# Optimization experiments

Measured on AMD Instinct MI355X. Metric: run time of the kernel, lower is better.

Reference implementation:

```python
import jax, jax.numpy as jnp
import numpy as np

B_SZ, L_SEQ, H_CH, N_ST = 8, 4096, 256, 64


def setup_inputs() -> dict:
    key = jax.random.key(0)
    ks = jax.random.split(key, 12)
    rn = lambda k, s, sc=1.0: jax.random.normal(k, s, jnp.float32) * sc
    inp = {
        'x': rn(ks[0], (B_SZ, L_SEQ, H_CH)),
        # stable DPLR spectrum: Re(Lambda) < 0, HiPPO-like imaginary ladder
        'Lambda_re': -(jnp.abs(rn(ks[1], (N_ST,))) + 0.1),
        'Lambda_im': jnp.pi * jnp.arange(N_ST, dtype=jnp.float32),
        'P_re': rn(ks[2], (N_ST,), N_ST ** -0.5),
        'P_im': rn(ks[3], (N_ST,), N_ST ** -0.5),
        'Q_re': rn(ks[4], (N_ST,), N_ST ** -0.5),
        'Q_im': rn(ks[5], (N_ST,), N_ST ** -0.5),
        'B_re': rn(ks[6], (N_ST,), N_ST ** -0.5),
        'B_im': rn(ks[7], (N_ST,), N_ST ** -0.5),
        'C_re': rn(ks[8], (H_CH, N_ST), N_ST ** -0.5),
        'C_im': rn(ks[9], (H_CH, N_ST), N_ST ** -0.5),
        'step': jnp.ones((1,), jnp.float32) * 1e-3,
        'D': jnp.zeros((1,), jnp.float32),
        'W_fc': rn(ks[10], (H_CH, H_CH), H_CH ** -0.5),
        'b_fc': jnp.zeros((H_CH,), jnp.float32),
        'ln_g': jnp.ones((H_CH,), jnp.float32),
        'ln_b': jnp.zeros((H_CH,), jnp.float32),
    }
    return inp


def _dplr_kernel(Lambda_re, Lambda_im, P_re, P_im, Q_re, Q_im, B_re, B_im, C_re, C_im, step, L):
    # S4 DPLR generating function evaluated at the L roots of unity (torch_get_K_derta).
    Lam = (Lambda_re + 1j * Lambda_im).astype(jnp.complex64)  # (N,)
    Pc = (P_re + 1j * P_im).astype(jnp.complex64)
    Qc = (Q_re + 1j * Q_im).astype(jnp.complex64)
    Bc = (B_re + 1j * B_im).astype(jnp.complex64)
    Cc = (C_re + 1j * C_im).astype(jnp.complex64)  # (H, N)
    k = jnp.arange(L, dtype=jnp.float32)
    Omega = jnp.exp((-2j * jnp.pi) * (k / L)).astype(jnp.complex64)  # (L,)
    c = 2.0 / (1.0 + Omega)
    g = (2.0 / step[0]) * (1.0 - Omega) / (1.0 + Omega)  # bilinear transform points, (L,)
    inv = 1.0 / (g[:, None] - Lam[None, :])  # Cauchy matrix, (L, N)
    k00 = jnp.einsum('hn,ln->hl', Cc * Bc[None, :], inv)  # (H, L)
    k01 = jnp.einsum('hn,ln->hl', Cc * Pc[None, :], inv)
    k10 = jnp.einsum('n,ln->l', Qc * Bc, inv)  # (L,)
    k11 = jnp.einsum('n,ln->l', Qc * Pc, inv)
    atRoots = c[None, :] * (k00 - k01 * (k10 / (1.0 + k11))[None, :])  # Woodbury correction
    K = jnp.fft.ifft(atRoots, axis=-1).real  # (H, L)
    return K.astype(jnp.float32)


def reference(x, Lambda_re, Lambda_im, P_re, P_im, Q_re, Q_im, B_re, B_im, C_re, C_im, step, D, W_fc, b_fc, ln_g, ln_b):
    Bsz, L, H = x.shape
    step = jnp.maximum(step, 1e-6)
    K = _dplr_kernel(Lambda_re, Lambda_im, P_re, P_im, Q_re, Q_im, B_re, B_im, C_re, C_im, step, L)  # (H, L)
    # causal FFT convolution per channel (torch_convolution with fft=True)
    n = 2 * L
    Kf = jnp.fft.rfft(K, n=n, axis=-1)           # (H, F)
    uf = jnp.fft.rfft(x, n=n, axis=1)            # (B, F, H)
    h1 = jnp.fft.irfft(uf * Kf.T[None], n=n, axis=1)[:, :L, :]
    y1 = jax.nn.gelu(h1 + D * x, approximate=False)  # mult_activation='gelu'
    y2 = jax.nn.gelu(y1 @ W_fc.T + b_fc, approximate=False)  # fc + final_act
    y2 = y2 + x  # skip
    mu = jnp.mean(y2, axis=-1, keepdims=True)
    var = jnp.var(y2, axis=-1, keepdims=True)
    y = (y2 - mu) / jnp.sqrt(var + 1e-5) * ln_g + ln_b  # LayerNorm; dropout p=0
    h_ratio = jnp.max(jnp.abs(y), axis=1) / (jnp.max(jnp.abs(x), axis=1) + 1e-6)  # (B, H)
    return y, h_ratio
```

## Files before the change

kernel.cpp:

```cpp
#include <hip/hip_runtime.h>
#include <math.h>

#define TPB 256

typedef float2 cf;
typedef __attribute__((ext_vector_type(8))) short bf16x8;
typedef __attribute__((ext_vector_type(4))) float f32x4;

__device__ __forceinline__ cf cmk(float x, float y){ cf r; r.x=x; r.y=y; return r; }
__device__ __forceinline__ cf cml(cf a, cf b){ return cmk(a.x*b.x - a.y*b.y, a.x*b.y + a.y*b.x); }
__device__ __forceinline__ cf cad(cf a, cf b){ return cmk(a.x+b.x, a.y+b.y); }
__device__ __forceinline__ cf csb(cf a, cf b){ return cmk(a.x-b.x, a.y-b.y); }
__device__ __forceinline__ cf crcp(cf d){ float r = 1.0f/(d.x*d.x + d.y*d.y); return cmk(d.x*r, -d.y*r); }
__device__ __forceinline__ cf cdv(cf n, cf d){ return cml(n, crcp(d)); }
__device__ __forceinline__ float geluf(float z){ return 0.5f*z*(1.0f + erff(z*0.70710678118654752f)); }

__device__ __forceinline__ cf twid(float f, float sign){
  float h = f * 0.5f;
  float s = __builtin_amdgcn_sinf(h);
  float c0 = __builtin_amdgcn_cosf(h);
  return cmk(c0, sign * s);
}

__device__ __forceinline__ cf shflx(cf v, int m){
  return cmk(__shfl_xor(v.x, m), __shfl_xor(v.y, m));
}

__device__ __forceinline__ void bfsplit(float v, ushort* h, ushort* l){
  unsigned u = __float_as_uint(v);
  unsigned hr = (u + 0x7FFFu + ((u >> 16) & 1u)) & 0xFFFF0000u;
  *h = (ushort)(hr >> 16);
  float lv = v - __uint_as_float(hr);
  unsigned u2 = __float_as_uint(lv);
  *l = (ushort)((u2 + 0x7FFFu + ((u2 >> 16) & 1u)) >> 16);
}

__device__ __forceinline__ void dif4q(cf& q0, cf& q1, cf& q2, cf& q3, cf w1, float sign){
  cf w2 = cml(w1, w1);
  cf a1 = cad(q0, q2);
  cf c1 = cml(csb(q0, q2), w1);
  cf b1 = cad(q1, q3);
  cf d1 = cml(csb(q1, q3), cmk(-sign*w1.y, sign*w1.x));
  q0 = cad(a1, b1);
  q1 = cml(csb(a1, b1), w2);
  q2 = cad(c1, d1);
  q3 = cml(csb(c1, d1), w2);
}
__device__ __forceinline__ void dit4q(cf& q0, cf& q1, cf& q2, cf& q3, cf w1, float sign){
  cf w2 = cml(w1, w1);
  cf t1 = cml(q1, w2);
  cf a1 = cad(q0, t1), b1 = csb(q0, t1);
  cf t2 = cml(q3, w2);
  cf c1 = cad(q2, t2), d1 = csb(q2, t2);
  cf v1 = cml(c1, w1);
  cf v2 = cml(d1, cmk(-sign*w1.y, sign*w1.x));
  q0 = cad(a1, v1);
  q2 = csb(a1, v1);
  q1 = cad(b1, v2);
  q3 = csb(b1, v2);
}

template<int N, int SSTART>
__device__ void fft_dif_r4(cf* __restrict__ a, float sign){
  #pragma unroll
  for (int s = SSTART; s >= 1; s >>= 2){
    __syncthreads();
    #pragma unroll
    for (int g = 0; g < (N >> 2) / TPB; g++){
      int w = (int)threadIdx.x + g * TPB;
      int j = w & (s - 1);
      int base = ((w & ~(s - 1)) << 2) | j;
      cf A0 = a[base], B0 = a[base + s], C0 = a[base + 2*s], D0 = a[base + 3*s];
      cf w1 = twid((float)j / (float)(2 * s), sign);
      cf w2 = cml(w1, w1);
      cf a1 = cad(A0, C0);
      cf c1 = cml(csb(A0, C0), w1);
      cf b1 = cad(B0, D0);
      cf d1 = cml(csb(B0, D0), cmk(-sign * w1.y, sign * w1.x));
      a[base]         = cad(a1, b1);
      a[base + s]     = cml(csb(a1, b1), w2);
      a[base + 2*s]   = cad(c1, d1);
      a[base + 3*s]   = cml(csb(c1, d1), w2);
    }
  }
  if constexpr ((__builtin_ctz(N) & 1) == 1){
    __syncthreads();
    #pragma unroll
    for (int g = 0; g < (N >> 1) / TPB; g++){
      int w = (int)threadIdx.x + g * TPB;
      int i = w << 1;
      cf u = a[i], v = a[i + 1];
      a[i] = cad(u, v);
      a[i + 1] = csb(u, v);
    }
  }
  __syncthreads();
}

template<int N>
__device__ void fft_dit_r4(cf* __restrict__ a, float sign){
  if constexpr ((__builtin_ctz(N) & 1) == 1){
    __syncthreads();
    #pragma unroll
    for (int g = 0; g < (N >> 1) / TPB; g++){
      int w = (int)threadIdx.x + g * TPB;
      int i = w << 1;
      cf u = a[i], v = a[i + 1];
      a[i] = cad(u, v);
      a[i + 1] = csb(u, v);
    }
  }
  constexpr int S0 = ((__builtin_ctz(N) & 1) == 1) ? 2 : 1;
  #pragma unroll
  for (int s = S0; s <= (N >> 2); s <<= 2){
    __syncthreads();
    #pragma unroll
    for (int g = 0; g < (N >> 2) / TPB; g++){
      int w = (int)threadIdx.x + g * TPB;
      int j = w & (s - 1);
      int base = ((w & ~(s - 1)) << 2) | j;
      cf A0 = a[base], B0 = a[base + s], C0 = a[base + 2*s], D0 = a[base + 3*s];
      cf w1 = twid((float)j / (float)(2 * s), sign);
      cf w2 = cml(w1, w1);
      cf t1 = cml(B0, w2);
      cf a1 = cad(A0, t1), b1 = csb(A0, t1);
      cf t2 = cml(D0, w2);
      cf c1 = cad(C0, t2), d1 = csb(C0, t2);
      cf v1 = cml(c1, w1);
      cf v2 = cml(d1, cmk(-sign * w1.y, sign * w1.x));
      a[base]         = cad(a1, v1);
      a[base + 2*s]   = csb(a1, v1);
      a[base + s]     = cad(b1, v2);
      a[base + 3*s]   = csb(b1, v2);
    }
  }
  __syncthreads();
}

__device__ void dif8192_pad_stage(cf* __restrict__ a, float sign){
  __syncthreads();
  #pragma unroll
  for (int g = 0; g < 8; g++){
    int w = (int)threadIdx.x + g * TPB;
    cf A0 = a[w], B0 = a[w + 2048];
    cf w1 = twid((float)w * (1.0f / 4096.0f), sign);
    cf w2 = cml(w1, w1);
    cf c1 = cml(A0, w1);
    cf d1 = cml(B0, cmk(-sign * w1.y, sign * w1.x));
    a[w]        = cad(A0, B0);
    a[w + 2048] = cml(csb(A0, B0), w2);
    a[w + 4096] = cad(c1, d1);
    a[w + 6144] = cml(csb(c1, d1), w2);
  }
}

__device__ __forceinline__ int brev13(int x){ return (int)(__brev((unsigned)x) >> 19); }

__global__ void k_init(unsigned* xmax, unsigned* ymax){
  int i = blockIdx.x * 256 + threadIdx.x;
  if (i < 2048){ xmax[i] = 0u; ymax[i] = 0u; }
}

__global__ __launch_bounds__(256) void k_transpose_x(const float* __restrict__ x,
                                                     float* __restrict__ xT,
                                                     unsigned* __restrict__ xmax){
  __shared__ float tile[64][65];
  __shared__ float red[64][4];
  int b = blockIdx.z;
  int t0 = blockIdx.x * 64;
  int h0 = blockIdx.y * 64;
  int hc = threadIdx.x & 63, tg = threadIdx.x >> 6;
  float pmax = 0.0f;
  #pragma unroll
  for (int q = 0; q < 16; q++){
    int tr = tg + q * 4;
    float v = x[((size_t)(b * 4096 + t0 + tr)) * 256 + h0 + hc];
    tile[tr][hc] = v;
    pmax = fmaxf(pmax, fabsf(v));
  }
  red[hc][tg] = pmax;
  __syncthreads();
  if (threadIdx.x < 64){
    float m = fmaxf(fmaxf(red[threadIdx.x][0], red[threadIdx.x][1]),
                    fmaxf(red[threadIdx.x][2], red[threadIdx.x][3]));
    atomicMax(&xmax[b * 256 + h0 + threadIdx.x], __float_as_uint(m));
  }
  #pragma unroll
  for (int q = 0; q < 16; q++){
    int hr = tg + q * 4;
    xT[((size_t)(b * 256 + h0 + hr)) * 4096 + t0 + hc] = tile[hc][hr];
  }
}

__global__ void k_wsplit(const float* __restrict__ W, ushort* __restrict__ Wh, ushort* __restrict__ Wl){
  int i = blockIdx.x * 256 + threadIdx.x;
  ushort h, l;
  bfsplit(W[i], &h, &l);
  Wh[i] = h; Wl[i] = l;
}

__global__ __launch_bounds__(256) void k_cauchy(
    const float* __restrict__ Lr, const float* __restrict__ Li,
    const float* __restrict__ Pr, const float* __restrict__ Pi,
    const float* __restrict__ Qr, const float* __restrict__ Qi,
    const float* __restrict__ Br, const float* __restrict__ Bi,
    const float* __restrict__ Cr, const float* __restrict__ Ci,
    const float* __restrict__ stepp, cf* __restrict__ A)
{
  __shared__ cf sLam[64], sB[64], sP[64], sQB[64], sQP[64];
  __shared__ cf sInv[64][16];
  __shared__ cf sWood[16], sC[16], sG[16];
  int tid = threadIdx.x;
  int l0 = blockIdx.x * 16;
  float stepv = fmaxf(stepp[0], 1e-6f);
  if (tid < 64){
    cf lam = cmk(Lr[tid], Li[tid]);
    cf b = cmk(Br[tid], Bi[tid]);
    cf p = cmk(Pr[tid], Pi[tid]);
    cf q = cmk(Qr[tid], Qi[tid]);
    sLam[tid] = lam; sB[tid] = b; sP[tid] = p;
    sQB[tid] = cml(q, b);
    sQP[tid] = cml(q, p);
  }
  __syncthreads();
  if (tid < 16){
    int l = l0 + tid;
    float ang = -6.2831855f * ((float)l * (1.0f / 4096.0f));
    cf Om = cmk(cosf(ang), sinf(ang));
    cf den = cmk(1.0f + Om.x, Om.y);
    cf num = cmk(1.0f - Om.x, -Om.y);
    cf rden = crcp(den);
    sC[tid] = cml(cmk(2.0f, 0.0f), rden);
    cf g = cml(num, rden);
    float sc = 2.0f / stepv;
    sG[tid] = cmk(g.x * sc, g.y * sc);
  }
  __syncthreads();
  for (int it = tid; it < 1024; it += 256){
    int n = it >> 4, ll = it & 15;
    sInv[n][ll] = crcp(csb(sG[ll], sLam[n]));
  }
  __syncthreads();
  if (tid < 16){
    cf k10 = cmk(0,0), k11 = cmk(0,0);
    for (int n = 0; n < 64; n++){
      k10 = cad(k10, cml(sQB[n], sInv[n][tid]));
      k11 = cad(k11, cml(sQP[n], sInv[n][tid]));
    }
    sWood[tid] = cdv(k10, cmk(1.0f + k11.x, k11.y));
  }
  __syncthreads();
  int h = tid;
  cf a0[16], a1[16];
  #pragma unroll
  for (int ll = 0; ll < 16; ll++){ a0[ll] = cmk(0,0); a1[ll] = cmk(0,0); }
  for (int n = 0; n < 64; n++){
    cf cc = cmk(Cr[h * 64 + n], Ci[h * 64 + n]);
    cf cb = cml(cc, sB[n]);
    cf cp = cml(cc, sP[n]);
    #pragma unroll
    for (int ll = 0; ll < 16; ll++){
      cf iv = sInv[n][ll];
      a0[ll] = cad(a0[ll], cml(cb, iv));
      a1[ll] = cad(a1[ll], cml(cp, iv));
    }
  }
  cf* dst = A + (size_t)h * 4096 + l0;
  #pragma unroll
  for (int ll = 0; ll < 16; ll++){
    dst[ll] = cml(sC[ll], csb(a0[ll], cml(a1[ll], sWood[ll])));
  }
}

__global__ __launch_bounds__(256) void k_kf(const cf* __restrict__ A, float4* __restrict__ Sab){
  extern __shared__ cf c[];
  int hp = blockIdx.x, tid = threadIdx.x;
  const cf* a1p = A + (size_t)(2 * hp) * 4096;
  const cf* a2p = a1p + 4096;
  for (int l = tid; l < 4096; l += TPB){
    int r = (int)(__brev((unsigned)l) >> 20);
    cf u = a1p[l], v = a2p[l];
    c[r] = cmk(u.x - v.y, u.y + v.x);
  }
  fft_dit_r4<4096>(c, 1.0f);
  float k1[16], k2[16];
  #pragma unroll
  for (int q = 0; q < 16; q++){
    cf w = c[tid + q * 256];
    k1[q] = w.x * (1.0f / 4096.0f);
    k2[q] = w.y * (1.0f / 4096.0f);
  }
  __syncthreads();
  #pragma unroll
  for (int q = 0; q < 16; q++) c[tid + q * 256] = cmk(k1[q], k2[q]);
  dif8192_pad_stage(c, -1.0f);
  fft_dif_r4<8192, 512>(c, -1.0f);
  float4* rec = Sab + (size_t)hp * 4097;
  const float sc = 0.5f * 0.5f * (1.0f / 8192.0f);
  #pragma unroll
  for (int q8 = 0; q8 < 16; q8++){
    int t = tid + 256 * q8;
    int p = t << 1;
    int k = brev13(p);
    int qq = brev13((8192 - k) & 8191);
    cf Zp = c[p], Zq = c[qq];
    float K1x = (Zp.x + Zq.x), K1y = (Zp.y - Zq.y);
    float dx  = (Zp.x - Zq.x), dy  = (Zp.y + Zq.y);
    float K2x = dy, K2y = -dx;
    rec[t] = make_float4((K1x + K2x) * sc, (K1y + K2y) * sc,
                         (K1x - K2x) * sc, (K1y - K2y) * sc);
  }
  if (tid == 0){
    cf Z1 = c[1];
    float K1x = 2.0f * Z1.x, K2x = 2.0f * Z1.y;
    rec[4096] = make_float4((K1x + K2x) * sc, 0.0f, (K1x - K2x) * sc, 0.0f);
  }
}

__global__ __launch_bounds__(256) void k_conv(const float* __restrict__ xT,
                                              const float4* __restrict__ Sab,
                                              const float* __restrict__ Dp,
                                              ushort* __restrict__ y1h,
                                              ushort* __restrict__ y1l){
  __shared__ cf c[8320];
  int blk = blockIdx.x;
  int b = blk >> 7, hp = blk & 127;
  int t = threadIdx.x;
  const float* xs1 = xT + ((size_t)(b * 256 + 2 * hp)) * 4096;
  const float* xs2 = xs1 + 4096;
  cf v[32];
  #pragma unroll
  for (int r = 0; r < 16; r++){
    int n = t + 256 * r;
    v[r] = cmk(xs1[n], xs2[n]);
  }
  #pragma unroll
  for (int r = 0; r < 16; r++)
    v[r + 16] = cml(v[r], twid((float)(t + 256 * r) * (1.0f / 4096.0f), -1.0f));
  #pragma unroll
  for (int r0 = 0; r0 < 4; r0++){
    cf w1 = twid((float)(t + 256 * r0) * (1.0f / 2048.0f), -1.0f);
    dif4q(v[r0], v[r0 + 4], v[r0 + 8], v[r0 + 12], w1, -1.0f);
    dif4q(v[r0 + 16], v[r0 + 20], v[r0 + 24], v[r0 + 28], w1, -1.0f);
  }
  {
    cf w1 = twid((float)t * (1.0f / 512.0f), -1.0f);
    #pragma unroll
    for (int r = 0; r < 32; r += 4)
      dif4q(v[r], v[r + 1], v[r + 2], v[r + 3], w1, -1.0f);
  }
  #pragma unroll
  for (int r = 0; r < 32; r++) c[t + 260 * r] = v[r];
  __syncthreads();
  int Bq = t >> 3, sg = t & 7;
  int m1 = Bq * 260 + sg;
  #pragma unroll
  for (int u = 0; u < 32; u++) v[u] = c[m1 + 8 * u];
  #pragma unroll
  for (int u = 0; u < 8; u++){
    cf w1 = twid((float)(sg + 8 * u) * (1.0f / 128.0f), -1.0f);
    dif4q(v[u], v[u + 8], v[u + 16], v[u + 24], w1, -1.0f);
  }
  #pragma unroll
  for (int p2 = 0; p2 < 2; p2++){
    cf w1 = twid((float)(sg + 8 * p2) * (1.0f / 32.0f), -1.0f);
    #pragma unroll
    for (int u0 = 0; u0 < 32; u0 += 8)
      dif4q(v[u0 + p2], v[u0 + p2 + 2], v[u0 + p2 + 4], v[u0 + p2 + 6], w1, -1.0f);
  }
  {
    cf tw = twid((float)sg * (1.0f / 8.0f), -1.0f);
    #pragma unroll
    for (int u = 0; u < 32; u += 2){
      cf lo = cad(v[u], v[u + 1]);
      cf hi = cml(csb(v[u], v[u + 1]), tw);
      v[u] = lo; v[u + 1] = hi;
    }
  }
  {
    bool h4 = (sg & 4) != 0;
    cf tw4 = twid((float)(sg & 3) * 0.25f, -1.0f);
    #pragma unroll
    for (int u = 0; u < 32; u++){
      cf o = shflx(v[u], 4);
      v[u] = h4 ? cml(csb(o, v[u]), tw4) : cad(v[u], o);
    }
    bool h2 = (sg & 2) != 0;
    cf tw2 = twid((float)(sg & 1) * 0.5f, -1.0f);
    #pragma unroll
    for (int u = 0; u < 32; u++){
      cf o = shflx(v[u], 2);
      v[u] = h2 ? cml(csb(o, v[u]), tw2) : cad(v[u], o);
    }
    bool h1 = (sg & 1) != 0;
    #pragma unroll
    for (int u = 0; u < 32; u++){
      cf o = shflx(v[u], 1);
      v[u] = h1 ? csb(o, v[u]) : cad(v[u], o);
    }
  }
  #pragma unroll
  for (int u = 0; u < 32; u++) c[m1 + 8 * u] = v[u];
  __syncthreads();
  const float4* rec = Sab + (size_t)hp * 4097;
  #pragma unroll
  for (int q8 = 0; q8 < 16; q8++){
    int th = t + 256 * q8;
    int p = th << 1;
    int k = brev13(p);
    int qq = brev13((8192 - k) & 8191);
    int pi = p + 4 * (p >> 8), qi = qq + 4 * (qq >> 8);
    cf Zp = c[pi], Zq = c[qi];
    float4 r0 = rec[th];
    cf Sap = cmk(r0.x, r0.y), Sbp = cmk(r0.z, r0.w);
    cf cZq = cmk(Zq.x, -Zq.y), cZp = cmk(Zp.x, -Zp.y);
    c[pi] = cad(cml(Zp, Sap), cml(cZq, Sbp));
    cf cSa = cmk(Sap.x, -Sap.y), cSb = cmk(Sbp.x, -Sbp.y);
    c[qi] = cad(cml(Zq, cSa), cml(cZp, cSb));
  }
  if (t == 0){
    float4 e = rec[4096];
    cf Z1 = c[1];
    c[1] = cad(cml(Z1, cmk(e.x, e.y)), cml(cmk(Z1.x, -Z1.y), cmk(e.z, e.w)));
  }
  __syncthreads();
  #pragma unroll
  for (int u = 0; u < 32; u++) v[u] = c[m1 + 8 * u];
  {
    bool h1 = (sg & 1) != 0;
    #pragma unroll
    for (int u = 0; u < 32; u++){
      cf o = shflx(v[u], 1);
      v[u] = h1 ? csb(o, v[u]) : cad(v[u], o);
    }
    bool h2 = (sg & 2) != 0;
    cf w2 = twid((float)(sg & 1) * 0.5f, 1.0f);
    #pragma unroll
    for (int u = 0; u < 32; u++){
      cf o = shflx(v[u], 2);
      cf whv = cml(w2, h2 ? v[u] : o);
      v[u] = h2 ? csb(o, whv) : cad(v[u], whv);
    }
    bool h4 = (sg & 4) != 0;
    cf w4 = twid((float)(sg & 3) * 0.25f, 1.0f);
    #pragma unroll
    for (int u = 0; u < 32; u++){
      cf o = shflx(v[u], 4);
      cf whv = cml(w4, h4 ? v[u] : o);
      v[u] = h4 ? csb(o, whv) : cad(v[u], whv);
    }
  }
  {
    cf tw = twid((float)sg * (1.0f / 8.0f), 1.0f);
    #pragma unroll
    for (int u = 0; u < 32; u += 2){
      cf tb = cml(v[u + 1], tw);
      cf a = v[u];
      v[u] = cad(a, tb);
      v[u + 1] = csb(a, tb);
    }
  }
  #pragma unroll
  for (int p2 = 0; p2 < 2; p2++){
    cf w1 = twid((float)(sg + 8 * p2) * (1.0f / 32.0f), 1.0f);
    #pragma unroll
    for (int u0 = 0; u0 < 32; u0 += 8)
      dit4q(v[u0 + p2], v[u0 + p2 + 2], v[u0 + p2 + 4], v[u0 + p2 + 6], w1, 1.0f);
  }
  #pragma unroll
  for (int u = 0; u < 8; u++){
    cf w1 = twid((float)(sg + 8 * u) * (1.0f / 128.0f), 1.0f);
    dit4q(v[u], v[u + 8], v[u + 16], v[u + 24], w1, 1.0f);
  }
  #pragma unroll
  for (int u = 0; u < 32; u++) c[m1 + 8 * u] = v[u];
  __syncthreads();
  #pragma unroll
  for (int r = 0; r < 32; r++) v[r] = c[t + 260 * r];
  {
    cf tw = twid((float)t * (1.0f / 256.0f), 1.0f);
    #pragma unroll
    for (int r = 0; r < 32; r += 2){
      cf tb = cml(v[r + 1], tw);
      cf a = v[r];
      v[r] = cad(a, tb);
      v[r + 1] = csb(a, tb);
    }
  }
  #pragma unroll
  for (int p2 = 0; p2 < 2; p2++){
    cf w1 = twid((float)(t + 256 * p2) * (1.0f / 1024.0f), 1.0f);
    #pragma unroll
    for (int r0 = 0; r0 < 32; r0 += 8)
      dit4q(v[r0 + p2], v[r0 + p2 + 2], v[r0 + p2 + 4], v[r0 + p2 + 6], w1, 1.0f);
  }
  #pragma unroll
  for (int r0 = 0; r0 < 8; r0++){
    cf w1 = twid((float)(t + 256 * r0) * (1.0f / 4096.0f), 1.0f);
    dit4q(v[r0], v[r0 + 8], v[r0 + 16], v[r0 + 24], w1, 1.0f);
  }
  float Dv = Dp[0];
  size_t base = ((size_t)(b * 256 + 2 * hp)) * 4096;
  #pragma unroll
  for (int r = 0; r < 16; r++){
    int n = t + 256 * r;
    cf w = v[r];
    float z1 = geluf(fmaf(Dv, xs1[n], w.x));
    float z2 = geluf(fmaf(Dv, xs2[n], w.y));
    ushort h0, l0, h1u, l1;
    bfsplit(z1, &h0, &l0);
    bfsplit(z2, &h1u, &l1);
    y1h[base + n] = h0;        y1l[base + n] = l0;
    y1h[base + 4096 + n] = h1u; y1l[base + 4096 + n] = l1;
  }
}

__global__ __launch_bounds__(256, 3) void k_gemm_ln(
    const ushort* __restrict__ y1h, const ushort* __restrict__ y1l,
    const ushort* __restrict__ Wh, const ushort* __restrict__ Wl,
    const float* __restrict__ bfc, const float* __restrict__ x,
    const float* __restrict__ lng, const float* __restrict__ lnb,
    float* __restrict__ yout, unsigned* __restrict__ ymax)
{
  __shared__ ushort sY[2][64 * 40];
  __shared__ float red1[64][4], red2[64][4];
  int tid = threadIdx.x;
  int l = tid & 63;
  int w = tid >> 6;
  int blk = blockIdx.x;
  int b = blk >> 6;
  int t0 = (blk & 63) * 64;
  int g = l >> 4, cc = l & 15;

  f32x4 acc[4][4];
  #pragma unroll
  for (int m = 0; m < 4; m++)
    #pragma unroll
    for (int n = 0; n < 4; n++)
      acc[m][n] = (f32x4){0.0f, 0.0f, 0.0f, 0.0f};

  int kk = tid >> 3, ts = (tid & 7) * 8;

  #pragma unroll 1
  for (int kc = 0; kc < 256; kc += 32){
    __syncthreads();
    {
      size_t gb = ((size_t)(b * 256 + kc + kk)) * 4096 + t0 + ts;
      float4 vh = *(const float4*)(y1h + gb);
      float4 vl = *(const float4*)(y1l + gb);
      const ushort* ph = (const ushort*)&vh;
      const ushort* pl = (const ushort*)&vl;
      int kblk = kk >> 3, kin = kk & 7;
      #pragma unroll
      for (int e = 0; e < 8; e++){
        int t = ts + e;
        int idx = t * 40 + ((kblk ^ ((t >> 3) & 3)) << 3) + kin;
        sY[0][idx] = ph[e];
        sY[1][idx] = pl[e];
      }
    }
    __syncthreads();
    bf16x8 afh[4], afl[4];
    #pragma unroll
    for (int m = 0; m < 4; m++){
      int t = m * 16 + cc;
      int idx = t * 40 + ((g ^ ((t >> 3) & 3)) << 3);
      afh[m] = *(bf16x8*)&sY[0][idx];
      afl[m] = *(bf16x8*)&sY[1][idx];
    }
    #pragma unroll
    for (int n = 0; n < 4; n++){
      size_t wj = (size_t)(w * 64 + n * 16 + cc) * 256 + kc + g * 8;
      bf16x8 bh = *(const bf16x8*)(Wh + wj);
      bf16x8 bl = *(const bf16x8*)(Wl + wj);
      #pragma unroll
      for (int m = 0; m < 4; m++){
        acc[m][n] = __builtin_amdgcn_mfma_f32_16x16x32_bf16(afh[m], bh, acc[m][n], 0, 0, 0);
        acc[m][n] = __builtin_amdgcn_mfma_f32_16x16x32_bf16(afh[m], bl, acc[m][n], 0, 0, 0);
        acc[m][n] = __builtin_amdgcn_mfma_f32_16x16x32_bf16(afl[m], bh, acc[m][n], 0, 0, 0);
      }
    }
  }

  float bj[4], gj[4], lj[4];
  #pragma unroll
  for (int n = 0; n < 4; n++){
    int j = w * 64 + n * 16 + cc;
    bj[n] = bfc[j]; gj[n] = lng[j]; lj[n] = lnb[j];
  }
  #pragma unroll
  for (int m = 0; m < 4; m++){
    #pragma unroll
    for (int r = 0; r < 4; r++){
      int tl = m * 16 + g * 4 + r;
      size_t rowb = ((size_t)(b * 4096 + t0 + tl)) * 256;
      float ss = 0.0f, sq = 0.0f;
      #pragma unroll
      for (int n = 0; n < 4; n++){
        float z = geluf(acc[m][n][r] + bj[n]) + x[rowb + w * 64 + n * 16 + cc];
        acc[m][n][r] = z;
        ss += z; sq = fmaf(z, z, sq);
      }
      #pragma unroll
      for (int msk = 1; msk < 16; msk <<= 1){
        ss += __shfl_xor(ss, msk);
        sq += __shfl_xor(sq, msk);
      }
      if (cc == 0){ red1[tl][w] = ss; red2[tl][w] = sq; }
    }
  }
  __syncthreads();
  float jm[4] = {0.0f, 0.0f, 0.0f, 0.0f};
  #pragma unroll
  for (int m = 0; m < 4; m++){
    #pragma unroll
    for (int r = 0; r < 4; r++){
      int tl = m * 16 + g * 4 + r;
      float ts1 = red1[tl][0] + red1[tl][1] + red1[tl][2] + red1[tl][3];
      float ts2 = red2[tl][0] + red2[tl][1] + red2[tl][2] + red2[tl][3];
      float mu = ts1 * (1.0f / 256.0f);
      float var = ts2 * (1.0f / 256.0f) - mu * mu;
      float rstd = rsqrtf(var + 1e-5f);
      size_t rowb = ((size_t)(b * 4096 + t0 + tl)) * 256;
      #pragma unroll
      for (int n = 0; n < 4; n++){
        float yv = (acc[m][n][r] - mu) * rstd * gj[n] + lj[n];
        yout[rowb + w * 64 + n * 16 + cc] = yv;
        jm[n] = fmaxf(jm[n], fabsf(yv));
      }
    }
  }
  #pragma unroll
  for (int n = 0; n < 4; n++){
    jm[n] = fmaxf(jm[n], __shfl_xor(jm[n], 16));
    jm[n] = fmaxf(jm[n], __shfl_xor(jm[n], 32));
  }
  if (g == 0){
    #pragma unroll
    for (int n = 0; n < 4; n++)
      atomicMax(&ymax[b * 256 + w * 64 + n * 16 + cc], __float_as_uint(jm[n]));
  }
}

__global__ void k_ratio(const unsigned* __restrict__ ymax, const unsigned* __restrict__ xmax,
                        float* __restrict__ out){
  int i = blockIdx.x * 256 + threadIdx.x;
  if (i < 2048){
    float ym = __uint_as_float(ymax[i]);
    float xm = __uint_as_float(xmax[i]);
    out[8388608 + i] = ym / (xm + 1e-6f);
  }
}

extern "C" void kernel_launch(void* const* d_in, const int* in_sizes, int n_in,
                              void* d_out, int out_size, void* d_ws, size_t ws_size,
                              hipStream_t stream)
{
  const float* x    = (const float*)d_in[0];
  const float* Lr   = (const float*)d_in[1];
  const float* Li   = (const float*)d_in[2];
  const float* Pr   = (const float*)d_in[3];
  const float* Pi   = (const float*)d_in[4];
  const float* Qr   = (const float*)d_in[5];
  const float* Qi   = (const float*)d_in[6];
  const float* Br   = (const float*)d_in[7];
  const float* Bi   = (const float*)d_in[8];
  const float* Cr   = (const float*)d_in[9];
  const float* Ci   = (const float*)d_in[10];
  const float* stp  = (const float*)d_in[11];
  const float* Dp   = (const float*)d_in[12];
  const float* Wfc  = (const float*)d_in[13];
  const float* bfc  = (const float*)d_in[14];
  const float* lng  = (const float*)d_in[15];
  const float* lnb  = (const float*)d_in[16];

  char* ws = (char*)d_ws;
  float*    xT   = (float*)(ws);
  float4*   Sab  = (float4*)(ws + ((size_t)32 << 20));
  cf*       A    = (cf*)(ws + ((size_t)41 << 20));
  ushort*   y1h  = (ushort*)(ws + ((size_t)41 << 20));
  ushort*   y1l  = (ushort*)(ws + ((size_t)57 << 20));
  ushort*   Wh   = (ushort*)(ws + ((size_t)73 << 20));
  ushort*   Wl   = (ushort*)(ws + ((size_t)73 << 20) + (128u << 10));
  unsigned* xmax = (unsigned*)(ws + ((size_t)73 << 20) + (256u << 10));
  unsigned* ymax = xmax + 2048;

  k_init<<<8, 256, 0, stream>>>(xmax, ymax);
  dim3 gt(64, 4, 8);
  k_transpose_x<<<gt, 256, 0, stream>>>(x, xT, xmax);
  k_wsplit<<<256, 256, 0, stream>>>(Wfc, Wh, Wl);
  k_cauchy<<<256, 256, 0, stream>>>(Lr, Li, Pr, Pi, Qr, Qi, Br, Bi, Cr, Ci, stp, A);
  k_kf<<<128, 256, 65536, stream>>>(A, Sab);
  k_conv<<<1024, 256, 0, stream>>>(xT, Sab, Dp, y1h, y1l);
  k_gemm_ln<<<512, 256, 0, stream>>>(y1h, y1l, Wh, Wl, bfc, x, lng, lnb, (float*)d_out, ymax);
  k_ratio<<<8, 256, 0, stream>>>(ymax, xmax, (float*)d_out);
}
```

Baseline: 211.2 us.

## Double FFT block size to 512 threads and restructure conv FFT decomposition

The kernel-spectrum and convolution kernels move from 256 to 512 threads per block. Each thread now holds 16 complex values instead of 32. The conv kernel's 8192-point FFT is restructured: one radix-2 pass is folded into the final output twiddle, the shared-memory exchange uses 512-element padded rows, and five wavefront-shuffle butterfly stages replace three. The aims are lower register pressure, more waves per CU to hide latency, and fewer LDS round trips, at the cost of more shuffle traffic and a larger barrier scope.

```diff
diff --git a/kernel.cpp b/kernel.cpp
--- a/kernel.cpp
+++ b/kernel.cpp
@@ -1,7 +1,5 @@
 #include <hip/hip_runtime.h>
 #include <math.h>
-
-#define TPB 256
 
 typedef float2 cf;
 typedef __attribute__((ext_vector_type(8))) short bf16x8;
@@ -11,6 +9,7 @@
 __device__ __forceinline__ cf cml(cf a, cf b){ return cmk(a.x*b.x - a.y*b.y, a.x*b.y + a.y*b.x); }
 __device__ __forceinline__ cf cad(cf a, cf b){ return cmk(a.x+b.x, a.y+b.y); }
 __device__ __forceinline__ cf csb(cf a, cf b){ return cmk(a.x-b.x, a.y-b.y); }
+__device__ __forceinline__ cf cjg(cf a){ return cmk(a.x, -a.y); }
 __device__ __forceinline__ cf crcp(cf d){ float r = 1.0f/(d.x*d.x + d.y*d.y); return cmk(d.x*r, -d.y*r); }
 __device__ __forceinline__ cf cdv(cf n, cf d){ return cml(n, crcp(d)); }
 __device__ __forceinline__ float geluf(float z){ return 0.5f*z*(1.0f + erff(z*0.70710678118654752f)); }
@@ -60,14 +59,18 @@
   q3 = csb(b1, v2);
 }
 
-template<int N, int SSTART>
+__device__ __forceinline__ int brev12(int x){ return (int)(__brev((unsigned)x) >> 20); }
+__device__ __forceinline__ int brev13(int x){ return (int)(__brev((unsigned)x) >> 19); }
+__device__ __forceinline__ int pidx(int n){ return n + 4*(n>>8); }
+
+template<int N, int SSTART, int TP>
 __device__ void fft_dif_r4(cf* __restrict__ a, float sign){
   #pragma unroll
   for (int s = SSTART; s >= 1; s >>= 2){
     __syncthreads();
     #pragma unroll
-    for (int g = 0; g < (N >> 2) / TPB; g++){
-      int w = (int)threadIdx.x + g * TPB;
+    for (int g = 0; g < (N >> 2) / TP; g++){
+      int w = (int)threadIdx.x + g * TP;
       int j = w & (s - 1);
       int base = ((w & ~(s - 1)) << 2) | j;
       cf A0 = a[base], B0 = a[base + s], C0 = a[base + 2*s], D0 = a[base + 3*s];
@@ -86,8 +89,8 @@
   if constexpr ((__builtin_ctz(N) & 1) == 1){
     __syncthreads();
     #pragma unroll
-    for (int g = 0; g < (N >> 1) / TPB; g++){
-      int w = (int)threadIdx.x + g * TPB;
+    for (int g = 0; g < (N >> 1) / TP; g++){
+      int w = (int)threadIdx.x + g * TP;
       int i = w << 1;
       cf u = a[i], v = a[i + 1];
       a[i] = cad(u, v);
@@ -97,13 +100,13 @@
   __syncthreads();
 }
 
-template<int N>
+template<int N, int TP>
 __device__ void fft_dit_r4(cf* __restrict__ a, float sign){
   if constexpr ((__builtin_ctz(N) & 1) == 1){
     __syncthreads();
     #pragma unroll
-    for (int g = 0; g < (N >> 1) / TPB; g++){
-      int w = (int)threadIdx.x + g * TPB;
+    for (int g = 0; g < (N >> 1) / TP; g++){
+      int w = (int)threadIdx.x + g * TP;
       int i = w << 1;
       cf u = a[i], v = a[i + 1];
       a[i] = cad(u, v);
@@ -115,8 +118,8 @@
   for (int s = S0; s <= (N >> 2); s <<= 2){
     __syncthreads();
     #pragma unroll
-    for (int g = 0; g < (N >> 2) / TPB; g++){
-      int w = (int)threadIdx.x + g * TPB;
+    for (int g = 0; g < (N >> 2) / TP; g++){
+      int w = (int)threadIdx.x + g * TP;
       int j = w & (s - 1);
       int base = ((w & ~(s - 1)) << 2) | j;
       cf A0 = a[base], B0 = a[base + s], C0 = a[base + 2*s], D0 = a[base + 3*s];
@@ -137,11 +140,12 @@
   __syncthreads();
 }
 
+template<int TP>
 __device__ void dif8192_pad_stage(cf* __restrict__ a, float sign){
   __syncthreads();
   #pragma unroll
-  for (int g = 0; g < 8; g++){
-    int w = (int)threadIdx.x + g * TPB;
+  for (int g = 0; g < 2048 / TP; g++){
+    int w = (int)threadIdx.x + g * TP;
     cf A0 = a[w], B0 = a[w + 2048];
     cf w1 = twid((float)w * (1.0f / 4096.0f), sign);
     cf w2 = cml(w1, w1);
@@ -153,8 +157,6 @@
     a[w + 6144] = cml(csb(c1, d1), w2);
   }
 }
-
-__device__ __forceinline__ int brev13(int x){ return (int)(__brev((unsigned)x) >> 19); }
 
 __global__ void k_init(unsigned* xmax, unsigned* ymax){
   int i = blockIdx.x * 256 + threadIdx.x;
@@ -272,34 +274,34 @@
   }
 }
 
-__global__ __launch_bounds__(256) void k_kf(const cf* __restrict__ A, float4* __restrict__ Sab){
+__global__ __launch_bounds__(512) void k_kf(const cf* __restrict__ A, float4* __restrict__ Sab){
   extern __shared__ cf c[];
   int hp = blockIdx.x, tid = threadIdx.x;
   const cf* a1p = A + (size_t)(2 * hp) * 4096;
   const cf* a2p = a1p + 4096;
-  for (int l = tid; l < 4096; l += TPB){
-    int r = (int)(__brev((unsigned)l) >> 20);
-    cf u = a1p[l], v = a2p[l];
-    c[r] = cmk(u.x - v.y, u.y + v.x);
-  }
-  fft_dit_r4<4096>(c, 1.0f);
-  float k1[16], k2[16];
-  #pragma unroll
-  for (int q = 0; q < 16; q++){
-    cf w = c[tid + q * 256];
+  for (int l = tid; l < 4096; l += 512){
+    int r = brev12(l);
+    cf u = a1p[l], w = a2p[l];
+    c[r] = cmk(u.x - w.y, u.y + w.x);
+  }
+  fft_dit_r4<4096, 512>(c, 1.0f);
+  float k1[8], k2[8];
+  #pragma unroll
+  for (int q = 0; q < 8; q++){
+    cf w = c[tid + q * 512];
     k1[q] = w.x * (1.0f / 4096.0f);
     k2[q] = w.y * (1.0f / 4096.0f);
   }
   __syncthreads();
   #pragma unroll
-  for (int q = 0; q < 16; q++) c[tid + q * 256] = cmk(k1[q], k2[q]);
-  dif8192_pad_stage(c, -1.0f);
-  fft_dif_r4<8192, 512>(c, -1.0f);
+  for (int q = 0; q < 8; q++) c[tid + q * 512] = cmk(k1[q], k2[q]);
+  dif8192_pad_stage<512>(c, -1.0f);
+  fft_dif_r4<8192, 512, 512>(c, -1.0f);
   float4* rec = Sab + (size_t)hp * 4097;
   const float sc = 0.5f * 0.5f * (1.0f / 8192.0f);
   #pragma unroll
-  for (int q8 = 0; q8 < 16; q8++){
-    int t = tid + 256 * q8;
+  for (int q8 = 0; q8 < 8; q8++){
+    int t = tid + 512 * q8;
     int p = t << 1;
     int k = brev13(p);
     int qq = brev13((8192 - k) & 8191);
@@ -317,7 +319,7 @@
   }
 }
 
-__global__ __launch_bounds__(256) void k_conv(const float* __restrict__ xT,
+__global__ __launch_bounds__(512) void k_conv(const float* __restrict__ xT,
                                               const float4* __restrict__ Sab,
                                               const float* __restrict__ Dp,
                                               ushort* __restrict__ y1h,
@@ -326,191 +328,162 @@
   int blk = blockIdx.x;
   int b = blk >> 7, hp = blk & 127;
   int t = threadIdx.x;
+  int a = t >> 5, cl = t & 31;
   const float* xs1 = xT + ((size_t)(b * 256 + 2 * hp)) * 4096;
   const float* xs2 = xs1 + 4096;
-  cf v[32];
-  #pragma unroll
-  for (int r = 0; r < 16; r++){
-    int n = t + 256 * r;
+  cf v[16];
+  #pragma unroll
+  for (int r = 0; r < 8; r++){
+    int n = t + 512 * r;
     v[r] = cmk(xs1[n], xs2[n]);
   }
   #pragma unroll
-  for (int r = 0; r < 16; r++)
-    v[r + 16] = cml(v[r], twid((float)(t + 256 * r) * (1.0f / 4096.0f), -1.0f));
-  #pragma unroll
-  for (int r0 = 0; r0 < 4; r0++){
-    cf w1 = twid((float)(t + 256 * r0) * (1.0f / 2048.0f), -1.0f);
-    dif4q(v[r0], v[r0 + 4], v[r0 + 8], v[r0 + 12], w1, -1.0f);
-    dif4q(v[r0 + 16], v[r0 + 20], v[r0 + 24], v[r0 + 28], w1, -1.0f);
+  for (int r = 0; r < 8; r++)
+    v[r + 8] = cml(v[r], twid((float)(t + 512 * r) * (1.0f / 4096.0f), -1.0f));
+  #pragma unroll
+  for (int h = 0; h < 16; h += 8){
+    #pragma unroll
+    for (int r0 = 0; r0 < 2; r0++){
+      cf w1 = twid((float)(t + 512 * r0) * (1.0f / 2048.0f), -1.0f);
+      dif4q(v[h + r0], v[h + r0 + 2], v[h + r0 + 4], v[h + r0 + 6], w1, -1.0f);
+    }
   }
   {
-    cf w1 = twid((float)t * (1.0f / 512.0f), -1.0f);
-    #pragma unroll
-    for (int r = 0; r < 32; r += 4)
-      dif4q(v[r], v[r + 1], v[r + 2], v[r + 3], w1, -1.0f);
-  }
-  #pragma unroll
-  for (int r = 0; r < 32; r++) c[t + 260 * r] = v[r];
-  __syncthreads();
-  int Bq = t >> 3, sg = t & 7;
-  int m1 = Bq * 260 + sg;
-  #pragma unroll
-  for (int u = 0; u < 32; u++) v[u] = c[m1 + 8 * u];
-  #pragma unroll
-  for (int u = 0; u < 8; u++){
-    cf w1 = twid((float)(sg + 8 * u) * (1.0f / 128.0f), -1.0f);
-    dif4q(v[u], v[u + 8], v[u + 16], v[u + 24], w1, -1.0f);
-  }
-  #pragma unroll
-  for (int p2 = 0; p2 < 2; p2++){
-    cf w1 = twid((float)(sg + 8 * p2) * (1.0f / 32.0f), -1.0f);
-    #pragma unroll
-    for (int u0 = 0; u0 < 32; u0 += 8)
-      dif4q(v[u0 + p2], v[u0 + p2 + 2], v[u0 + p2 + 4], v[u0 + p2 + 6], w1, -1.0f);
+    cf tw = twid((float)t * (1.0f / 512.0f), -1.0f);
+    #pragma unroll
+    for (int r = 0; r < 16; r += 2){
+      cf lo = cad(v[r], v[r + 1]);
+      cf hi = cml(csb(v[r], v[r + 1]), tw);
+      v[r] = lo; v[r + 1] = hi;
+    }
+  }
+  __syncthreads();
+  #pragma unroll
+  for (int r = 0; r < 16; r++) c[pidx(t + 512 * r)] = v[r];
+  __syncthreads();
+  #pragma unroll
+  for (int u = 0; u < 16; u++) v[u] = c[pidx(a * 512 + u * 32 + cl)];
+  #pragma unroll
+  for (int u0 = 0; u0 < 4; u0++){
+    cf w1 = twid((float)(u0 * 32 + cl) * (1.0f / 256.0f), -1.0f);
+    dif4q(v[u0], v[u0 + 4], v[u0 + 8], v[u0 + 12], w1, -1.0f);
   }
   {
-    cf tw = twid((float)sg * (1.0f / 8.0f), -1.0f);
-    #pragma unroll
-    for (int u = 0; u < 32; u += 2){
-      cf lo = cad(v[u], v[u + 1]);
-      cf hi = cml(csb(v[u], v[u + 1]), tw);
-      v[u] = lo; v[u + 1] = hi;
+    cf w1 = twid((float)cl * (1.0f / 64.0f), -1.0f);
+    #pragma unroll
+    for (int g = 0; g < 16; g += 4)
+      dif4q(v[g], v[g + 1], v[g + 2], v[g + 3], w1, -1.0f);
+  }
+  #pragma unroll
+  for (int m = 16; m >= 2; m >>= 1){
+    bool hb = (cl & m) != 0;
+    cf tw = twid((float)(cl & (m - 1)) * (1.0f / (float)m), -1.0f);
+    #pragma unroll
+    for (int u = 0; u < 16; u++){
+      cf o = shflx(v[u], m);
+      v[u] = hb ? cml(csb(o, v[u]), tw) : cad(v[u], o);
     }
   }
   {
-    bool h4 = (sg & 4) != 0;
-    cf tw4 = twid((float)(sg & 3) * 0.25f, -1.0f);
-    #pragma unroll
-    for (int u = 0; u < 32; u++){
-      cf o = shflx(v[u], 4);
-      v[u] = h4 ? cml(csb(o, v[u]), tw4) : cad(v[u], o);
-    }
-    bool h2 = (sg & 2) != 0;
-    cf tw2 = twid((float)(sg & 1) * 0.5f, -1.0f);
-    #pragma unroll
-    for (int u = 0; u < 32; u++){
-      cf o = shflx(v[u], 2);
-      v[u] = h2 ? cml(csb(o, v[u]), tw2) : cad(v[u], o);
-    }
-    bool h1 = (sg & 1) != 0;
-    #pragma unroll
-    for (int u = 0; u < 32; u++){
+    bool hb = (cl & 1) != 0;
+    #pragma unroll
+    for (int u = 0; u < 16; u++){
       cf o = shflx(v[u], 1);
-      v[u] = h1 ? csb(o, v[u]) : cad(v[u], o);
-    }
-  }
-  #pragma unroll
-  for (int u = 0; u < 32; u++) c[m1 + 8 * u] = v[u];
-  __syncthreads();
-  const float4* rec = Sab + (size_t)hp * 4097;
-  #pragma unroll
-  for (int q8 = 0; q8 < 16; q8++){
-    int th = t + 256 * q8;
-    int p = th << 1;
-    int k = brev13(p);
-    int qq = brev13((8192 - k) & 8191);
-    int pi = p + 4 * (p >> 8), qi = qq + 4 * (qq >> 8);
-    cf Zp = c[pi], Zq = c[qi];
-    float4 r0 = rec[th];
-    cf Sap = cmk(r0.x, r0.y), Sbp = cmk(r0.z, r0.w);
-    cf cZq = cmk(Zq.x, -Zq.y), cZp = cmk(Zp.x, -Zp.y);
-    c[pi] = cad(cml(Zp, Sap), cml(cZq, Sbp));
-    cf cSa = cmk(Sap.x, -Sap.y), cSb = cmk(Sbp.x, -Sbp.y);
-    c[qi] = cad(cml(Zq, cSa), cml(cZp, cSb));
-  }
-  if (t == 0){
-    float4 e = rec[4096];
-    cf Z1 = c[1];
-    c[1] = cad(cml(Z1, cmk(e.x, e.y)), cml(cmk(Z1.x, -Z1.y), cmk(e.z, e.w)));
-  }
-  __syncthreads();
-  #pragma unroll
-  for (int u = 0; u < 32; u++) v[u] = c[m1 + 8 * u];
+      v[u] = hb ? csb(o, v[u]) : cad(v[u], o);
+    }
+  }
+  #pragma unroll
+  for (int u = 0; u < 16; u++) c[pidx(a * 512 + u * 32 + cl)] = v[u];
+  __syncthreads();
   {
-    bool h1 = (sg & 1) != 0;
-    #pragma unroll
-    for (int u = 0; u < 32; u++){
+    const float4* rec = Sab + (size_t)hp * 4097;
+    #pragma unroll
+    for (int q8 = 0; q8 < 8; q8++){
+      int th = t + 512 * q8;
+      int p = th << 1;
+      int k = brev13(p);
+      int qq = brev13((8192 - k) & 8191);
+      int pi = pidx(p), qi = pidx(qq);
+      cf Zp = c[pi], Zq = c[qi];
+      float4 r0 = rec[th];
+      cf Sap = cmk(r0.x, r0.y), Sbp = cmk(r0.z, r0.w);
+      c[pi] = cad(cml(Zp, Sap), cml(cjg(Zq), Sbp));
+      c[qi] = cad(cml(Zq, cjg(Sap)), cml(cjg(Zp), cjg(Sbp)));
+    }
+    if (t == 0){
+      float4 e = rec[4096];
+      cf Z1 = c[pidx(1)];
+      c[pidx(1)] = cad(cml(Z1, cmk(e.x, e.y)), cml(cjg(Z1), cmk(e.z, e.w)));
+    }
+  }
+  __syncthreads();
+  #pragma unroll
+  for (int u = 0; u < 16; u++) v[u] = c[pidx(a * 512 + u * 32 + cl)];
+  {
+    bool hb = (cl & 1) != 0;
+    #pragma unroll
+    for (int u = 0; u < 16; u++){
       cf o = shflx(v[u], 1);
-      v[u] = h1 ? csb(o, v[u]) : cad(v[u], o);
-    }
-    bool h2 = (sg & 2) != 0;
-    cf w2 = twid((float)(sg & 1) * 0.5f, 1.0f);
-    #pragma unroll
-    for (int u = 0; u < 32; u++){
-      cf o = shflx(v[u], 2);
-      cf whv = cml(w2, h2 ? v[u] : o);
-      v[u] = h2 ? csb(o, whv) : cad(v[u], whv);
-    }
-    bool h4 = (sg & 4) != 0;
-    cf w4 = twid((float)(sg & 3) * 0.25f, 1.0f);
-    #pragma unroll
-    for (int u = 0; u < 32; u++){
-      cf o = shflx(v[u], 4);
-      cf whv = cml(w4, h4 ? v[u] : o);
-      v[u] = h4 ? csb(o, whv) : cad(v[u], whv);
+      v[u] = hb ? csb(o, v[u]) : cad(v[u], o);
+    }
+  }
+  #pragma unroll
+  for (int m = 2; m <= 16; m <<= 1){
+    bool hb = (cl & m) != 0;
+    cf w = twid((float)(cl & (m - 1)) * (1.0f / (float)m), 1.0f);
+    #pragma unroll
+    for (int u = 0; u < 16; u++){
+      cf o = shflx(v[u], m);
+      cf whv = cml(w, hb ? v[u] : o);
+      v[u] = hb ? csb(o, whv) : cad(v[u], whv);
     }
   }
   {
-    cf tw = twid((float)sg * (1.0f / 8.0f), 1.0f);
-    #pragma unroll
-    for (int u = 0; u < 32; u += 2){
-      cf tb = cml(v[u + 1], tw);
-      cf a = v[u];
-      v[u] = cad(a, tb);
-      v[u + 1] = csb(a, tb);
-    }
-  }
-  #pragma unroll
-  for (int p2 = 0; p2 < 2; p2++){
-    cf w1 = twid((float)(sg + 8 * p2) * (1.0f / 32.0f), 1.0f);
-    #pragma unroll
-    for (int u0 = 0; u0 < 32; u0 += 8)
-      dit4q(v[u0 + p2], v[u0 + p2 + 2], v[u0 + p2 + 4], v[u0 + p2 + 6], w1, 1.0f);
-  }
-  #pragma unroll
-  for (int u = 0; u < 8; u++){
-    cf w1 = twid((float)(sg + 8 * u) * (1.0f / 128.0f), 1.0f);
-    dit4q(v[u], v[u + 8], v[u + 16], v[u + 24], w1, 1.0f);
-  }
-  #pragma unroll
-  for (int u = 0; u < 32; u++) c[m1 + 8 * u] = v[u];
-  __syncthreads();
-  #pragma unroll
-  for (int r = 0; r < 32; r++) v[r] = c[t + 260 * r];
+    cf w1 = twid((float)cl * (1.0f / 64.0f), 1.0f);
+    #pragma unroll
+    for (int g = 0; g < 16; g += 4)
+      dit4q(v[g], v[g + 1], v[g + 2], v[g + 3], w1, 1.0f);
+  }
+  #pragma unroll
+  for (int u0 = 0; u0 < 4; u0++){
+    cf w1 = twid((float)(u0 * 32 + cl) * (1.0f / 256.0f), 1.0f);
+    dit4q(v[u0], v[u0 + 4], v[u0 + 8], v[u0 + 12], w1, 1.0f);
+  }
+  #pragma unroll
+  for (int u = 0; u < 16; u++) c[pidx(a * 512 + u * 32 + cl)] = v[u];
+  __syncthreads();
+  #pragma unroll
+  for (int r = 0; r < 16; r++) v[r] = c[pidx(t + 512 * r)];
   {
-    cf tw = twid((float)t * (1.0f / 256.0f), 1.0f);
-    #pragma unroll
-    for (int r = 0; r < 32; r += 2){
+    cf tw = twid((float)t * (1.0f / 512.0f), 1.0f);
+    #pragma unroll
+    for (int r = 0; r < 16; r += 2){
       cf tb = cml(v[r + 1], tw);
-      cf a = v[r];
-      v[r] = cad(a, tb);
-      v[r + 1] = csb(a, tb);
-    }
-  }
-  #pragma unroll
-  for (int p2 = 0; p2 < 2; p2++){
-    cf w1 = twid((float)(t + 256 * p2) * (1.0f / 1024.0f), 1.0f);
-    #pragma unroll
-    for (int r0 = 0; r0 < 32; r0 += 8)
-      dit4q(v[r0 + p2], v[r0 + p2 + 2], v[r0 + p2 + 4], v[r0 + p2 + 6], w1, 1.0f);
-  }
-  #pragma unroll
-  for (int r0 = 0; r0 < 8; r0++){
-    cf w1 = twid((float)(t + 256 * r0) * (1.0f / 4096.0f), 1.0f);
-    dit4q(v[r0], v[r0 + 8], v[r0 + 16], v[r0 + 24], w1, 1.0f);
+      cf a0 = v[r];
+      v[r] = cad(a0, tb);
+      v[r + 1] = csb(a0, tb);
+    }
+  }
+  #pragma unroll
+  for (int h = 0; h < 16; h += 8){
+    #pragma unroll
+    for (int r0 = 0; r0 < 2; r0++){
+      cf w1 = twid((float)(t + 512 * r0) * (1.0f / 2048.0f), 1.0f);
+      dit4q(v[h + r0], v[h + r0 + 2], v[h + r0 + 4], v[h + r0 + 6], w1, 1.0f);
+    }
   }
   float Dv = Dp[0];
   size_t base = ((size_t)(b * 256 + 2 * hp)) * 4096;
   #pragma unroll
-  for (int r = 0; r < 16; r++){
-    int n = t + 256 * r;
-    cf w = v[r];
+  for (int r = 0; r < 8; r++){
+    int n = t + 512 * r;
+    cf w = cad(v[r], cml(v[r + 8], twid((float)n * (1.0f / 4096.0f), 1.0f)));
     float z1 = geluf(fmaf(Dv, xs1[n], w.x));
     float z2 = geluf(fmaf(Dv, xs2[n], w.y));
     ushort h0, l0, h1u, l1;
     bfsplit(z1, &h0, &l0);
     bfsplit(z2, &h1u, &l1);
-    y1h[base + n] = h0;        y1l[base + n] = l0;
+    y1h[base + n] = h0;         y1l[base + n] = l0;
     y1h[base + 4096 + n] = h1u; y1l[base + 4096 + n] = l1;
   }
 }
@@ -690,8 +663,8 @@
   k_transpose_x<<<gt, 256, 0, stream>>>(x, xT, xmax);
   k_wsplit<<<256, 256, 0, stream>>>(Wfc, Wh, Wl);
   k_cauchy<<<256, 256, 0, stream>>>(Lr, Li, Pr, Pi, Qr, Qi, Br, Bi, Cr, Ci, stp, A);
-  k_kf<<<128, 256, 65536, stream>>>(A, Sab);
-  k_conv<<<1024, 256, 0, stream>>>(xT, Sab, Dp, y1h, y1l);
+  k_kf<<<128, 512, 65536, stream>>>(A, Sab);
+  k_conv<<<1024, 512, 0, stream>>>(xT, Sab, Dp, y1h, y1l);
   k_gemm_ln<<<512, 256, 0, stream>>>(y1h, y1l, Wh, Wl, bfc, x, lng, lnb, (float*)d_out, ymax);
   k_ratio<<<8, 256, 0, stream>>>(ymax, xmax, (float*)d_out);
 }
```

New measurement: 213.8 us. Within noise of the previous version (+1.3%).
